# Optimization experiments

Hardware: AMD Instinct MI355X
Metric: run time of the kernel (lower is better)

The kernel has to match this reference:

```python
import jax, jax.numpy as jnp
import numpy as np

MASK_THRESHOLD = 0.01
HOTSPOT_PERCENTILE = 90.0
ALPHA = 0.5
EPS = 1e-08


def setup_inputs() -> dict:
    key = jax.random.key(0)
    k1, k2 = jax.random.split(key)
    shape = (8, 1, 128, 128, 128)  # [B, 1, D, H, W]
    pred = jax.random.uniform(k1, shape, dtype=jnp.float32)
    target = jax.random.uniform(k2, shape, dtype=jnp.float32)
    return {"pred": pred, "target": target}


def _masked_quantile(v, q):
    """Quantile (linear interpolation, matching torch.quantile) over entries v > 0.
    Falls back to MASK_THRESHOLD when no valid entries exist."""
    vv = jnp.where(v > 0, v, jnp.nan)
    th = jnp.nanquantile(vv, q)  # ignores nan entries, linear interpolation
    return jnp.where(jnp.isnan(th), jnp.asarray(MASK_THRESHOLD, v.dtype), th)


def _dice_loss_single(p, t, m):
    # p, t, m: [1, D, H, W] for one batch element
    masked_target = (t * m).ravel()
    masked_pred = (p * m).ravel()
    q = HOTSPOT_PERCENTILE / 100.0
    target_threshold = _masked_quantile(masked_target, q)
    pred_threshold = _masked_quantile(masked_pred, q)
    target_hot = (masked_target > target_threshold).astype(p.dtype)
    pred_hot = (masked_pred > pred_threshold).astype(p.dtype)
    intersection = jnp.sum(pred_hot * target_hot)
    union = jnp.sum(pred_hot) + jnp.sum(target_hot) + EPS
    return 1.0 - 2.0 * intersection / union


def reference(pred, target):
    mask = (target > MASK_THRESHOLD).astype(pred.dtype)  # [B,1,D,H,W]
    squared_error = (pred - target) ** 2 * mask
    num_valid = jnp.sum(mask, axis=(1, 2, 3, 4)) + EPS  # [B]
    mse_loss = jnp.sum(squared_error, axis=(1, 2, 3, 4)) / num_valid  # [B]
    dice_loss = jax.vmap(_dice_loss_single)(pred, target, mask)  # [B]
    combined = ALPHA * mse_loss + (1.0 - ALPHA) * dice_loss
    return jnp.mean(combined)  # reduction='mean'
```

## Files before the change

### kernel.cpp

```cpp
#include <hip/hip_runtime.h>

#define NBINS 2048
#define BPB   64
#define TPB   256
#define NB    8
#define LCAP  512
#define PCAP  8192
#define SCAP  4096

static __device__ __forceinline__ unsigned bucketOf(float v) {
    unsigned b = (unsigned)(v * (float)NBINS);
    return b > (NBINS - 1) ? (NBINS - 1) : b;
}

static __device__ __forceinline__ void gload4(float4& d, const float4* a) {
    asm volatile("global_load_dwordx4 %0, %1, off" : "=v"(d) : "v"(a));
}
#define WAIT_VMCNT(N)                                              \
    do {                                                           \
        asm volatile("s_waitcnt vmcnt(" #N ")" ::: "memory");      \
        __builtin_amdgcn_sched_barrier(0);                         \
    } while (0)

#define ISSUE(SET, c)                                              \
    do {                                                           \
        const float4* tb_ = t4 + i0 + (c) * 4 * S;                 \
        const float4* pb_ = p4 + i0 + (c) * 4 * S;                 \
        gload4(t##SET##0, tb_);         gload4(t##SET##1, tb_ + S);      \
        gload4(t##SET##2, tb_ + 2 * S); gload4(t##SET##3, tb_ + 3 * S);  \
        gload4(p##SET##0, pb_);         gload4(p##SET##1, pb_ + S);      \
        gload4(p##SET##2, pb_ + 2 * S); gload4(p##SET##3, pb_ + 3 * S);  \
    } while (0)

__global__ __launch_bounds__(TPB) void k_pass1(const float* __restrict__ pred,
                                               const float* __restrict__ targ,
                                               int nvec,
                                               unsigned short* __restrict__ hist16,
                                               double* __restrict__ sse,
                                               unsigned* __restrict__ nvalid)
{
    __shared__ unsigned h[2 * NBINS];
    for (int k = threadIdx.x; k < 2 * NBINS; k += TPB) h[k] = 0u;
    __syncthreads();

    const int b = blockIdx.y;
    const float4* __restrict__ p4 = (const float4*)pred + (size_t)b * nvec;
    const float4* __restrict__ t4 = (const float4*)targ + (size_t)b * nvec;

    float    lsse = 0.f;
    unsigned lnv = 0, lnp = 0;
    const int S  = BPB * TPB;
    const int i0 = blockIdx.x * TPB + threadIdx.x;

#define PEL1(tq, pq)                                             \
    {                                                            \
        float tv[4] = {tq.x, tq.y, tq.z, tq.w};                  \
        float pv[4] = {pq.x, pq.y, pq.z, pq.w};                  \
        _Pragma("unroll")                                        \
        for (int j = 0; j < 4; ++j) {                            \
            float tt = tv[j], pp = pv[j];                        \
            if (tt > 0.01f) {                                    \
                float d = pp - tt;                               \
                lsse += d * d; lnv++;                            \
                atomicAdd(&h[bucketOf(tt)], 1u);                 \
                if (pp > 0.f) {                                  \
                    lnp++;                                       \
                    atomicAdd(&h[NBINS + bucketOf(pp)], 1u);     \
                }                                                \
            }                                                    \
        }                                                        \
    }
#define PROC1(SET)                                               \
    {                                                            \
        PEL1(t##SET##0, p##SET##0); PEL1(t##SET##1, p##SET##1);  \
        PEL1(t##SET##2, p##SET##2); PEL1(t##SET##3, p##SET##3);  \
    }

    float4 tA0, tA1, tA2, tA3, pA0, pA1, pA2, pA3;
    float4 tB0, tB1, tB2, tB3, pB0, pB1, pB2, pB3;

    ISSUE(A, 0);
    ISSUE(B, 1); WAIT_VMCNT(8); PROC1(A);
    ISSUE(A, 2); WAIT_VMCNT(8); PROC1(B);
    ISSUE(B, 3); WAIT_VMCNT(8); PROC1(A);
    ISSUE(A, 4); WAIT_VMCNT(8); PROC1(B);
    ISSUE(B, 5); WAIT_VMCNT(8); PROC1(A);
    ISSUE(A, 6); WAIT_VMCNT(8); PROC1(B);
    ISSUE(B, 7); WAIT_VMCNT(8); PROC1(A);
    WAIT_VMCNT(0); PROC1(B);
#undef PROC1
#undef PEL1
    __syncthreads();

    unsigned short* gh = hist16 + ((size_t)b * BPB + blockIdx.x) * (2 * NBINS);
    ushort4* gh4 = (ushort4*)gh;
    for (int k = threadIdx.x; k < (2 * NBINS) / 4; k += TPB) {
        ushort4 v;
        v.x = (unsigned short)h[4 * k + 0];
        v.y = (unsigned short)h[4 * k + 1];
        v.z = (unsigned short)h[4 * k + 2];
        v.w = (unsigned short)h[4 * k + 3];
        gh4[k] = v;
    }

    for (int off = 32; off; off >>= 1) {
        lsse += __shfl_down(lsse, off);
        lnv  += __shfl_down(lnv, off);
        lnp  += __shfl_down(lnp, off);
    }
    if ((threadIdx.x & 63) == 0) {
        atomicAdd(&sse[b], (double)lsse);
        atomicAdd(&nvalid[2 * b + 0], lnv);
        atomicAdd(&nvalid[2 * b + 1], lnp);
    }
}

__global__ __launch_bounds__(256) void k_scan(const unsigned short* __restrict__ hist16,
                                              const unsigned* __restrict__ nvalid,
                                              unsigned* __restrict__ binfo)
{
    const int bt = blockIdx.x;
    const int b = bt >> 1, t = bt & 1;
    const unsigned nv = nvalid[bt];
    unsigned* bi = binfo + bt * 8;

    __shared__ unsigned partial[256];
    __shared__ unsigned sk, sr2;

    if (threadIdx.x == 0) {
        bi[5] = nv;
        if (nv == 0) {
            bi[0] = 0xFFFFFFFFu; bi[1] = 0xFFFFFFFFu;
            bi[2] = 0; bi[3] = 0; bi[4] = __float_as_uint(0.0f);
        } else {
            double pos  = 0.9 * (double)(nv - 1);
            unsigned k  = (unsigned)pos;
            double frac = pos - (double)k;
            bi[3] = k;
            bi[4] = __float_as_uint((float)frac);
            sk = k;
            sr2 = (k + 2 <= nv) ? (k + 2) : (k + 1);
        }
    }
    __syncthreads();
    if (nv == 0) return;

    const unsigned r1 = sk + 1, r2 = sr2;

    const int lo = threadIdx.x * (NBINS / 256);
    unsigned local[NBINS / 256];
#pragma unroll
    for (int j = 0; j < NBINS / 256; ++j) local[j] = 0;
    for (int rep = 0; rep < BPB; ++rep) {
        const ushort4* h4 = (const ushort4*)(hist16 +
            ((size_t)b * BPB + rep) * (2 * NBINS) + (size_t)t * NBINS + lo);
        ushort4 a = h4[0], c = h4[1];
        local[0] += a.x; local[1] += a.y; local[2] += a.z; local[3] += a.w;
        local[4] += c.x; local[5] += c.y; local[6] += c.z; local[7] += c.w;
    }
    unsigned ls = 0;
#pragma unroll
    for (int j = 0; j < NBINS / 256; ++j) ls += local[j];

    partial[threadIdx.x] = ls;
    __syncthreads();
    for (int off = 1; off < 256; off <<= 1) {
        unsigned v = (threadIdx.x >= (unsigned)off) ? partial[threadIdx.x - off] : 0u;
        __syncthreads();
        partial[threadIdx.x] += v;
        __syncthreads();
    }
    unsigned run = partial[threadIdx.x] - ls;

#pragma unroll
    for (int j = 0; j < NBINS / 256; ++j) {
        unsigned c = local[j];
        if (c) {
            if (run < r1 && run + c >= r1) { bi[0] = lo + j; bi[2] = run; }
            if (run < r2 && run + c >= r2) { bi[1] = lo + j; }
        }
        run += c;
    }
}

__global__ __launch_bounds__(TPB) void k_pass2(const float* __restrict__ pred,
                                               const float* __restrict__ targ,
                                               int nvec,
                                               const unsigned* __restrict__ binfo,
                                               unsigned* __restrict__ npairs,
                                               unsigned* __restrict__ naa,
                                               float2* __restrict__ pairs)
{
    __shared__ float2   sbuf[LCAP];
    __shared__ unsigned scnt, sbase;
    if (threadIdx.x == 0) scnt = 0;
    __syncthreads();

    const int b = blockIdx.y;
    const unsigned lo_t = binfo[(2 * b + 0) * 8 + 0], hi_t = binfo[(2 * b + 0) * 8 + 1];
    const unsigned lo_p = binfo[(2 * b + 1) * 8 + 0], hi_p = binfo[(2 * b + 1) * 8 + 1];

    const float4* __restrict__ p4 = (const float4*)pred + (size_t)b * nvec;
    const float4* __restrict__ t4 = (const float4*)targ + (size_t)b * nvec;

    unsigned laa = 0;
    const int S  = BPB * TPB;
    const int i0 = blockIdx.x * TPB + threadIdx.x;

#define PEL2(tq, pq)                                                      \
    {                                                                     \
        float tv[4] = {tq.x, tq.y, tq.z, tq.w};                           \
        float pv[4] = {pq.x, pq.y, pq.z, pq.w};                           \
        _Pragma("unroll")                                                 \
        for (int j = 0; j < 4; ++j) {                                     \
            float tt = tv[j], pp = pv[j];                                 \
            if (tt > 0.01f) {                                             \
                unsigned at = bucketOf(tt);                               \
                bool t_in = (at >= lo_t) && (at <= hi_t);                 \
                bool t_ab = (at > hi_t);                                  \
                bool ppos = (pp > 0.f);                                   \
                unsigned ap = bucketOf(pp);                               \
                bool p_in = ppos && (ap >= lo_p) && (ap <= hi_p);         \
                bool p_ab = ppos && (ap > hi_p);                          \
                if (t_ab && p_ab) laa++;                                  \
                if (t_in || p_in) {                                       \
                    unsigned idx = atomicAdd(&scnt, 1u);                  \
                    if (idx < LCAP) sbuf[idx] = make_float2(tt, pp);      \
                }                                                         \
            }                                                             \
        }                                                                 \
    }
#define PROC2(SET)                                               \
    {                                                            \
        PEL2(t##SET##0, p##SET##0); PEL2(t##SET##1, p##SET##1);  \
        PEL2(t##SET##2, p##SET##2); PEL2(t##SET##3, p##SET##3);  \
    }

    float4 tA0, tA1, tA2, tA3, pA0, pA1, pA2, pA3;
    float4 tB0, tB1, tB2, tB3, pB0, pB1, pB2, pB3;

    ISSUE(A, 0);
    ISSUE(B, 1); WAIT_VMCNT(8); PROC2(A);
    ISSUE(A, 2); WAIT_VMCNT(8); PROC2(B);
    ISSUE(B, 3); WAIT_VMCNT(8); PROC2(A);
    ISSUE(A, 4); WAIT_VMCNT(8); PROC2(B);
    ISSUE(B, 5); WAIT_VMCNT(8); PROC2(A);
    ISSUE(A, 6); WAIT_VMCNT(8); PROC2(B);
    ISSUE(B, 7); WAIT_VMCNT(8); PROC2(A);
    WAIT_VMCNT(0); PROC2(B);
#undef PROC2
#undef PEL2
    __syncthreads();
    if (threadIdx.x == 0) {
        unsigned n = scnt < LCAP ? scnt : LCAP;
        sbase = atomicAdd(&npairs[b], n);
        scnt = n;
    }
    __syncthreads();
    for (unsigned k = threadIdx.x; k < scnt; k += TPB) {
        unsigned idx = sbase + k;
        if (idx < PCAP) pairs[(size_t)b * PCAP + idx] = sbuf[k];
    }
    for (int off = 32; off; off >>= 1) laa += __shfl_down(laa, off);
    if ((threadIdx.x & 63) == 0 && laa) atomicAdd(&naa[b], laa);
}

__global__ __launch_bounds__(1024) void k_sortsel(const unsigned* __restrict__ binfo,
                                                  const unsigned* __restrict__ npairs,
                                                  const float2* __restrict__ pairs,
                                                  float* __restrict__ thr,
                                                  unsigned* __restrict__ hotc)
{
    __shared__ float s[SCAP];
    __shared__ unsigned scnt, sle;
    __shared__ float sth;

    const int bt = blockIdx.x;
    const int b = bt >> 1, t = bt & 1;
    const unsigned* bi = binfo + bt * 8;
    const unsigned nv = bi[5];
    if (nv == 0) {
        if (threadIdx.x == 0) { thr[bt] = 0.01f; hotc[bt] = 0; }
        return;
    }
    const unsigned lo = bi[0], hi = bi[1];
    if (threadIdx.x == 0) { scnt = 0; sle = 0; }
    __syncthreads();

    unsigned np = npairs[b]; if (np > PCAP) np = PCAP;
    for (unsigned i = threadIdx.x; i < np; i += 1024) {
        float2 pr = pairs[(size_t)b * PCAP + i];
        float v = t ? pr.y : pr.x;
        if (v > 0.f) {
            unsigned a = bucketOf(v);
            if (a >= lo && a <= hi) {
                unsigned idx = atomicAdd(&scnt, 1u);
                if (idx < SCAP) s[idx] = v;
            }
        }
    }
    __syncthreads();
    unsigned n = scnt < SCAP ? scnt : SCAP;
    unsigned sn = 1; while (sn < n) sn <<= 1;
    if (sn < 2) sn = 2;
    for (unsigned i = n + threadIdx.x; i < sn; i += 1024) s[i] = 3.402823466e+38f;
    __syncthreads();

    for (unsigned ksz = 2; ksz <= sn; ksz <<= 1) {
        for (unsigned j = ksz >> 1; j; j >>= 1) {
            for (unsigned i = threadIdx.x; i < sn; i += 1024) {
                unsigned ixj = i ^ j;
                if (ixj > i) {
                    float a = s[i], c = s[ixj];
                    bool up = ((i & ksz) == 0);
                    if ((a > c) == up) { s[i] = c; s[ixj] = a; }
                }
            }
            __syncthreads();
        }
    }

    if (threadIdx.x == 0) {
        unsigned k = bi[3], cb = bi[2];
        float frac = __uint_as_float(bi[4]);
        long idx = (long)k - (long)cb;
        if (idx < 0) idx = 0;
        if (idx >= (long)n) idx = (long)n - 1;
        float v0 = s[idx];
        float v1 = (idx + 1 < (long)n) ? s[idx + 1] : v0;
        sth = v0 + frac * (v1 - v0);
        thr[bt] = sth;
    }
    __syncthreads();
    float th = sth;
    unsigned cle = 0;
    for (unsigned i = threadIdx.x; i < n; i += 1024) if (s[i] <= th) cle++;
    for (int off = 32; off; off >>= 1) cle += __shfl_down(cle, off);
    if ((threadIdx.x & 63) == 0 && cle) atomicAdd(&sle, cle);
    __syncthreads();
    if (threadIdx.x == 0) {
        unsigned gle = bi[2] + sle;
        hotc[bt] = nv - gle;
    }
}

__global__ __launch_bounds__(256) void k_final(const double* __restrict__ sse,
                                               const unsigned* __restrict__ nvalid,
                                               const unsigned* __restrict__ naa,
                                               const unsigned* __restrict__ npairs,
                                               const float2* __restrict__ pairs,
                                               const float* __restrict__ thr,
                                               const unsigned* __restrict__ hotc,
                                               float* __restrict__ out)
{
    __shared__ unsigned sI;
    __shared__ double acc;
    if (threadIdx.x == 0) acc = 0.0;
    for (int b = 0; b < NB; ++b) {
        if (threadIdx.x == 0) sI = 0;
        __syncthreads();
        float th_t = thr[2 * b + 0], th_p = thr[2 * b + 1];
        unsigned np = npairs[b]; if (np > PCAP) np = PCAP;
        unsigned c = 0;
        for (unsigned i = threadIdx.x; i < np; i += 256) {
            float2 pr = pairs[(size_t)b * PCAP + i];
            if (pr.x > th_t && pr.y > th_p) c++;
        }
        for (int off = 32; off; off >>= 1) c += __shfl_down(c, off);
        if ((threadIdx.x & 63) == 0 && c) atomicAdd(&sI, c);
        __syncthreads();
        if (threadIdx.x == 0) {
            double nv  = (double)nvalid[2 * b + 0];
            double mse = sse[b] / (nv + 1e-8);
            double T = (double)hotc[2 * b + 0];
            double P = (double)hotc[2 * b + 1];
            double I = (double)(naa[b] + sI);
            double dice = 1.0 - 2.0 * I / (P + T + 1e-8);
            acc += 0.5 * mse + 0.5 * dice;
        }
        __syncthreads();
    }
    if (threadIdx.x == 0) out[0] = (float)(acc / (double)NB);
}

extern "C" void kernel_launch(void* const* d_in, const int* in_sizes, int n_in,
                              void* d_out, int out_size, void* d_ws, size_t ws_size,
                              hipStream_t stream) {
    const float* pred = (const float*)d_in[0];
    const float* targ = (const float*)d_in[1];
    float* out = (float*)d_out;

    const int total = in_sizes[0];
    const int N     = total / NB;
    const int nvec  = N / 4;

    char* ws = (char*)d_ws;
    unsigned short* hist16 = (unsigned short*)(ws + 0);
    double*   sse    = (double*)  (ws + 4194304);
    unsigned* nvalid = (unsigned*)(ws + 4194368);
    unsigned* naa    = (unsigned*)(ws + 4194432);
    unsigned* npairs = (unsigned*)(ws + 4194496);
    unsigned* binfo  = (unsigned*)(ws + 4194560);
    float*    thr    = (float*)   (ws + 4195072);
    unsigned* hotc   = (unsigned*)(ws + 4195136);
    float2*   pairs  = (float2*)  (ws + 4195200);
    (void)ws_size; (void)n_in; (void)out_size;

    hipMemsetAsync(ws + 4194304, 0, 256, stream);

    dim3 gs(BPB, NB);
    k_pass1  <<<gs, TPB, 0, stream>>>(pred, targ, nvec, hist16, sse, nvalid);
    k_scan   <<<2 * NB, 256, 0, stream>>>(hist16, nvalid, binfo);
    k_pass2  <<<gs, TPB, 0, stream>>>(pred, targ, nvec, binfo, npairs, naa, pairs);
    k_sortsel<<<2 * NB, 1024, 0, stream>>>(binfo, npairs, pairs, thr, hotc);
    k_final  <<<1, 256, 0, stream>>>(sse, nvalid, naa, npairs, pairs, thr, hotc, out);
}
```

Baseline: 180.6 us.

## Speculate quantile window to fuse histogram and compaction into one pass

Replaces the histogram pass plus the compaction pass with a single pass. That pass counts elements below, inside and above a fixed value window around the expected 90th percentile and compacts the in-window pairs. A check kernel confirms that the quantile rank falls inside the window. Otherwise the original histogram, scan and compaction path runs as a fallback, so correctness holds for any input. This removes one full read of both input volumes in the common case, at the cost of extra small kernel launches, a guessed window, and a larger pair buffer.

```diff
diff --git a/kernel.cpp b/kernel.cpp
--- a/kernel.cpp
+++ b/kernel.cpp
@@ -4,9 +4,15 @@
 #define BPB   64
 #define TPB   256
 #define NB    8
-#define LCAP  512
-#define PCAP  8192
-#define SCAP  4096
+
+#define WLO 0.89453125f
+#define WHI 0.90673828125f
+
+#define PCAP  57344
+#define LCAP  1536
+#define FB_PCAP 8192
+#define FB_LCAP 512
+#define CCAP  512
 
 static __device__ __forceinline__ unsigned bucketOf(float v) {
     unsigned b = (unsigned)(v * (float)NBINS);
@@ -22,25 +28,39 @@
         __builtin_amdgcn_sched_barrier(0);                         \
     } while (0)
 
-#define ISSUE(SET, c)                                              \
-    do {                                                           \
-        const float4* tb_ = t4 + i0 + (c) * 4 * S;                 \
-        const float4* pb_ = p4 + i0 + (c) * 4 * S;                 \
+#define ISSUE(SET, c)                                                    \
+    do {                                                                 \
+        const float4* tb_ = t4 + i0 + (c) * 4 * S;                       \
+        const float4* pb_ = p4 + i0 + (c) * 4 * S;                       \
         gload4(t##SET##0, tb_);         gload4(t##SET##1, tb_ + S);      \
         gload4(t##SET##2, tb_ + 2 * S); gload4(t##SET##3, tb_ + 3 * S);  \
         gload4(p##SET##0, pb_);         gload4(p##SET##1, pb_ + S);      \
         gload4(p##SET##2, pb_ + 2 * S); gload4(p##SET##3, pb_ + 3 * S);  \
     } while (0)
 
-__global__ __launch_bounds__(TPB) void k_pass1(const float* __restrict__ pred,
-                                               const float* __restrict__ targ,
-                                               int nvec,
-                                               unsigned short* __restrict__ hist16,
-                                               double* __restrict__ sse,
-                                               unsigned* __restrict__ nvalid)
-{
-    __shared__ unsigned h[2 * NBINS];
-    for (int k = threadIdx.x; k < 2 * NBINS; k += TPB) h[k] = 0u;
+#define PIPELINE8(PROC)                      \
+    ISSUE(A, 0);                             \
+    ISSUE(B, 1); WAIT_VMCNT(8); PROC(A);     \
+    ISSUE(A, 2); WAIT_VMCNT(8); PROC(B);     \
+    ISSUE(B, 3); WAIT_VMCNT(8); PROC(A);     \
+    ISSUE(A, 4); WAIT_VMCNT(8); PROC(B);     \
+    ISSUE(B, 5); WAIT_VMCNT(8); PROC(A);     \
+    ISSUE(A, 6); WAIT_VMCNT(8); PROC(B);     \
+    ISSUE(B, 7); WAIT_VMCNT(8); PROC(A);     \
+    WAIT_VMCNT(0); PROC(B);
+
+
+__global__ __launch_bounds__(TPB) void k_main(const float* __restrict__ pred,
+                                              const float* __restrict__ targ,
+                                              int nvec,
+                                              double* __restrict__ sse,
+                                              unsigned* __restrict__ cnt,
+                                              unsigned* __restrict__ oflow,
+                                              float2* __restrict__ pairs)
+{
+    __shared__ float2   sbuf[LCAP];
+    __shared__ unsigned scnt, sbase;
+    if (threadIdx.x == 0) scnt = 0;
     __syncthreads();
 
     const int b = blockIdx.y;
@@ -48,11 +68,139 @@
     const float4* __restrict__ t4 = (const float4*)targ + (size_t)b * nvec;
 
     float    lsse = 0.f;
-    unsigned lnv = 0, lnp = 0;
+    unsigned lnvt = 0, lnvp = 0, linwt = 0, linwp = 0, labvt = 0, labvp = 0, lnaa = 0;
     const int S  = BPB * TPB;
     const int i0 = blockIdx.x * TPB + threadIdx.x;
 
-#define PEL1(tq, pq)                                             \
+#define PELM(tq, pq)                                                         \
+    {                                                                        \
+        float tv[4] = {tq.x, tq.y, tq.z, tq.w};                              \
+        float pv[4] = {pq.x, pq.y, pq.z, pq.w};                              \
+        _Pragma("unroll")                                                    \
+        for (int j = 0; j < 4; ++j) {                                        \
+            float tt = tv[j], pp = pv[j];                                    \
+            if (tt > 0.01f) {                                                \
+                float d = pp - tt;                                           \
+                lsse += d * d; lnvt++;                                       \
+                bool pz = (pp > 0.f); if (pz) lnvp++;                        \
+                bool tin = (tt >= WLO) && (tt < WHI);                        \
+                bool pin = pz && (pp >= WLO) && (pp < WHI);                  \
+                bool tab = (tt >= WHI);                                      \
+                bool pab = (pp >= WHI);                                      \
+                if (tin) linwt++;                                            \
+                if (pin) linwp++;                                            \
+                if (tab) labvt++;                                            \
+                if (pab) labvp++;                                            \
+                if (tab && pab) lnaa++;                                      \
+                if (tin || pin) {                                            \
+                    unsigned idx = atomicAdd(&scnt, 1u);                     \
+                    if (idx < LCAP) sbuf[idx] = make_float2(tt, pp);         \
+                }                                                            \
+            }                                                                \
+        }                                                                    \
+    }
+#define PROCM(SET)                                               \
+    {                                                            \
+        PELM(t##SET##0, p##SET##0); PELM(t##SET##1, p##SET##1);  \
+        PELM(t##SET##2, p##SET##2); PELM(t##SET##3, p##SET##3);  \
+    }
+
+    float4 tA0, tA1, tA2, tA3, pA0, pA1, pA2, pA3;
+    float4 tB0, tB1, tB2, tB3, pB0, pB1, pB2, pB3;
+    PIPELINE8(PROCM)
+#undef PROCM
+#undef PELM
+    __syncthreads();
+
+    if (threadIdx.x == 0) {
+        unsigned n = scnt;
+        if (n > LCAP) { atomicOr(oflow, 1u); n = LCAP; }
+        sbase = atomicAdd(&cnt[b * 8 + 7], n);
+        scnt = n;
+    }
+    __syncthreads();
+    for (unsigned k = threadIdx.x; k < scnt; k += TPB) {
+        unsigned idx = sbase + k;
+        if (idx < PCAP) pairs[(size_t)b * PCAP + idx] = sbuf[k];
+    }
+
+    for (int off = 32; off; off >>= 1) {
+        lsse  += __shfl_down(lsse, off);
+        lnvt  += __shfl_down(lnvt, off);
+        lnvp  += __shfl_down(lnvp, off);
+        linwt += __shfl_down(linwt, off);
+        linwp += __shfl_down(linwp, off);
+        labvt += __shfl_down(labvt, off);
+        labvp += __shfl_down(labvp, off);
+        lnaa  += __shfl_down(lnaa, off);
+    }
+    if ((threadIdx.x & 63) == 0) {
+        atomicAdd(&sse[b], (double)lsse);
+        atomicAdd(&cnt[b * 8 + 0], lnvt);
+        atomicAdd(&cnt[b * 8 + 1], lnvp);
+        atomicAdd(&cnt[b * 8 + 2], linwt);
+        atomicAdd(&cnt[b * 8 + 3], linwp);
+        atomicAdd(&cnt[b * 8 + 4], labvt);
+        atomicAdd(&cnt[b * 8 + 5], labvp);
+        atomicAdd(&cnt[b * 8 + 6], lnaa);
+    }
+}
+
+__global__ __launch_bounds__(64) void k_check(const unsigned* __restrict__ cnt,
+                                              const unsigned* __restrict__ oflow,
+                                              unsigned* __restrict__ sinfo)
+{
+    __shared__ unsigned okarr[16];
+    const int bt = threadIdx.x;
+    if (bt < 16) {
+        const int b = bt >> 1, t = bt & 1;
+        unsigned nv  = cnt[b * 8 + t];
+        unsigned inW = cnt[b * 8 + 2 + t];
+        unsigned abv = cnt[b * 8 + 4 + t];
+        unsigned below = nv - inW - abv;
+        unsigned ok = 0, k = 0; float frac = 0.f;
+        if (nv > 0 && inW > 0) {
+            double pos = 0.9 * (double)(nv - 1);
+            k = (unsigned)pos;
+            frac = (float)(pos - (double)k);
+            if (k >= below && (k + 1) <= below + inW - 1) ok = 1;
+        }
+        if (cnt[b * 8 + 7] > PCAP) ok = 0;
+        if (*oflow) ok = 0;
+        unsigned* si = sinfo + 8 + bt * 8;
+        si[0] = k;
+        si[1] = __float_as_uint(frac);
+        si[2] = below;
+        si[3] = nv;
+        si[4] = abv;
+        okarr[bt] = ok;
+    }
+    __syncthreads();
+    if (threadIdx.x == 0) {
+        unsigned ok = 1;
+        for (int i = 0; i < 16; ++i) ok &= okarr[i];
+        sinfo[0] = ok;
+    }
+}
+
+__global__ __launch_bounds__(TPB) void k_hist_fb(const float* __restrict__ pred,
+                                                 const float* __restrict__ targ,
+                                                 int nvec,
+                                                 const unsigned* __restrict__ sinfo,
+                                                 unsigned short* __restrict__ hist16)
+{
+    if (sinfo[0]) return;
+    __shared__ unsigned h[2 * NBINS];
+    for (int k = threadIdx.x; k < 2 * NBINS; k += TPB) h[k] = 0u;
+    __syncthreads();
+
+    const int b = blockIdx.y;
+    const float4* __restrict__ p4 = (const float4*)pred + (size_t)b * nvec;
+    const float4* __restrict__ t4 = (const float4*)targ + (size_t)b * nvec;
+    const int S  = BPB * TPB;
+    const int i0 = blockIdx.x * TPB + threadIdx.x;
+
+#define PELH(tq, pq)                                             \
     {                                                            \
         float tv[4] = {tq.x, tq.y, tq.z, tq.w};                  \
         float pv[4] = {pq.x, pq.y, pq.z, pq.w};                  \
@@ -60,36 +208,22 @@
         for (int j = 0; j < 4; ++j) {                            \
             float tt = tv[j], pp = pv[j];                        \
             if (tt > 0.01f) {                                    \
-                float d = pp - tt;                               \
-                lsse += d * d; lnv++;                            \
                 atomicAdd(&h[bucketOf(tt)], 1u);                 \
-                if (pp > 0.f) {                                  \
-                    lnp++;                                       \
+                if (pp > 0.f)                                    \
                     atomicAdd(&h[NBINS + bucketOf(pp)], 1u);     \
-                }                                                \
             }                                                    \
         }                                                        \
     }
-#define PROC1(SET)                                               \
+#define PROCH(SET)                                               \
     {                                                            \
-        PEL1(t##SET##0, p##SET##0); PEL1(t##SET##1, p##SET##1);  \
-        PEL1(t##SET##2, p##SET##2); PEL1(t##SET##3, p##SET##3);  \
-    }
-
+        PELH(t##SET##0, p##SET##0); PELH(t##SET##1, p##SET##1);  \
+        PELH(t##SET##2, p##SET##2); PELH(t##SET##3, p##SET##3);  \
+    }
     float4 tA0, tA1, tA2, tA3, pA0, pA1, pA2, pA3;
     float4 tB0, tB1, tB2, tB3, pB0, pB1, pB2, pB3;
-
-    ISSUE(A, 0);
-    ISSUE(B, 1); WAIT_VMCNT(8); PROC1(A);
-    ISSUE(A, 2); WAIT_VMCNT(8); PROC1(B);
-    ISSUE(B, 3); WAIT_VMCNT(8); PROC1(A);
-    ISSUE(A, 4); WAIT_VMCNT(8); PROC1(B);
-    ISSUE(B, 5); WAIT_VMCNT(8); PROC1(A);
-    ISSUE(A, 6); WAIT_VMCNT(8); PROC1(B);
-    ISSUE(B, 7); WAIT_VMCNT(8); PROC1(A);
-    WAIT_VMCNT(0); PROC1(B);
-#undef PROC1
-#undef PEL1
+    PIPELINE8(PROCH)
+#undef PROCH
+#undef PELH
     __syncthreads();
 
     unsigned short* gh = hist16 + ((size_t)b * BPB + blockIdx.x) * (2 * NBINS);
@@ -102,26 +236,17 @@
         v.w = (unsigned short)h[4 * k + 3];
         gh4[k] = v;
     }
-
-    for (int off = 32; off; off >>= 1) {
-        lsse += __shfl_down(lsse, off);
-        lnv  += __shfl_down(lnv, off);
-        lnp  += __shfl_down(lnp, off);
-    }
-    if ((threadIdx.x & 63) == 0) {
-        atomicAdd(&sse[b], (double)lsse);
-        atomicAdd(&nvalid[2 * b + 0], lnv);
-        atomicAdd(&nvalid[2 * b + 1], lnp);
-    }
-}
-
-__global__ __launch_bounds__(256) void k_scan(const unsigned short* __restrict__ hist16,
-                                              const unsigned* __restrict__ nvalid,
-                                              unsigned* __restrict__ binfo)
-{
+}
+
+__global__ __launch_bounds__(256) void k_scan_fb(const unsigned short* __restrict__ hist16,
+                                                 const unsigned* __restrict__ cnt,
+                                                 const unsigned* __restrict__ sinfo,
+                                                 unsigned* __restrict__ binfo)
+{
+    if (sinfo[0]) return;
     const int bt = blockIdx.x;
     const int b = bt >> 1, t = bt & 1;
-    const unsigned nv = nvalid[bt];
+    const unsigned nv = cnt[b * 8 + t];
     unsigned* bi = binfo + bt * 8;
 
     __shared__ unsigned partial[256];
@@ -135,9 +260,8 @@
         } else {
             double pos  = 0.9 * (double)(nv - 1);
             unsigned k  = (unsigned)pos;
-            double frac = pos - (double)k;
             bi[3] = k;
-            bi[4] = __float_as_uint((float)frac);
+            bi[4] = __float_as_uint((float)(pos - (double)k));
             sk = k;
             sr2 = (k + 2 <= nv) ? (k + 2) : (k + 1);
         }
@@ -146,7 +270,6 @@
     if (nv == 0) return;
 
     const unsigned r1 = sk + 1, r2 = sr2;
-
     const int lo = threadIdx.x * (NBINS / 256);
     unsigned local[NBINS / 256];
 #pragma unroll
@@ -161,7 +284,6 @@
     unsigned ls = 0;
 #pragma unroll
     for (int j = 0; j < NBINS / 256; ++j) ls += local[j];
-
     partial[threadIdx.x] = ls;
     __syncthreads();
     for (int off = 1; off < 256; off <<= 1) {
@@ -171,7 +293,6 @@
         __syncthreads();
     }
     unsigned run = partial[threadIdx.x] - ls;
-
 #pragma unroll
     for (int j = 0; j < NBINS / 256; ++j) {
         unsigned c = local[j];
@@ -183,15 +304,17 @@
     }
 }
 
-__global__ __launch_bounds__(TPB) void k_pass2(const float* __restrict__ pred,
-                                               const float* __restrict__ targ,
-                                               int nvec,
-                                               const unsigned* __restrict__ binfo,
-                                               unsigned* __restrict__ npairs,
-                                               unsigned* __restrict__ naa,
-                                               float2* __restrict__ pairs)
-{
-    __shared__ float2   sbuf[LCAP];
+__global__ __launch_bounds__(TPB) void k_compact_fb(const float* __restrict__ pred,
+                                                    const float* __restrict__ targ,
+                                                    int nvec,
+                                                    const unsigned* __restrict__ sinfo,
+                                                    const unsigned* __restrict__ binfo,
+                                                    unsigned* __restrict__ fb_npairs,
+                                                    unsigned* __restrict__ fb_naa,
+                                                    float2* __restrict__ fb_pairs)
+{
+    if (sinfo[0]) return;
+    __shared__ float2   sbuf[FB_LCAP];
     __shared__ unsigned scnt, sbase;
     if (threadIdx.x == 0) scnt = 0;
     __syncthreads();
@@ -202,12 +325,11 @@
 
     const float4* __restrict__ p4 = (const float4*)pred + (size_t)b * nvec;
     const float4* __restrict__ t4 = (const float4*)targ + (size_t)b * nvec;
-
     unsigned laa = 0;
     const int S  = BPB * TPB;
     const int i0 = blockIdx.x * TPB + threadIdx.x;
 
-#define PEL2(tq, pq)                                                      \
+#define PELC(tq, pq)                                                      \
     {                                                                     \
         float tv[4] = {tq.x, tq.y, tq.z, tq.w};                           \
         float pv[4] = {pq.x, pq.y, pq.z, pq.w};                           \
@@ -225,162 +347,228 @@
                 if (t_ab && p_ab) laa++;                                  \
                 if (t_in || p_in) {                                       \
                     unsigned idx = atomicAdd(&scnt, 1u);                  \
-                    if (idx < LCAP) sbuf[idx] = make_float2(tt, pp);      \
+                    if (idx < FB_LCAP) sbuf[idx] = make_float2(tt, pp);   \
                 }                                                         \
             }                                                             \
         }                                                                 \
     }
-#define PROC2(SET)                                               \
+#define PROCC(SET)                                               \
     {                                                            \
-        PEL2(t##SET##0, p##SET##0); PEL2(t##SET##1, p##SET##1);  \
-        PEL2(t##SET##2, p##SET##2); PEL2(t##SET##3, p##SET##3);  \
-    }
-
+        PELC(t##SET##0, p##SET##0); PELC(t##SET##1, p##SET##1);  \
+        PELC(t##SET##2, p##SET##2); PELC(t##SET##3, p##SET##3);  \
+    }
     float4 tA0, tA1, tA2, tA3, pA0, pA1, pA2, pA3;
     float4 tB0, tB1, tB2, tB3, pB0, pB1, pB2, pB3;
-
-    ISSUE(A, 0);
-    ISSUE(B, 1); WAIT_VMCNT(8); PROC2(A);
-    ISSUE(A, 2); WAIT_VMCNT(8); PROC2(B);
-    ISSUE(B, 3); WAIT_VMCNT(8); PROC2(A);
-    ISSUE(A, 4); WAIT_VMCNT(8); PROC2(B);
-    ISSUE(B, 5); WAIT_VMCNT(8); PROC2(A);
-    ISSUE(A, 6); WAIT_VMCNT(8); PROC2(B);
-    ISSUE(B, 7); WAIT_VMCNT(8); PROC2(A);
-    WAIT_VMCNT(0); PROC2(B);
-#undef PROC2
-#undef PEL2
+    PIPELINE8(PROCC)
+#undef PROCC
+#undef PELC
     __syncthreads();
     if (threadIdx.x == 0) {
-        unsigned n = scnt < LCAP ? scnt : LCAP;
-        sbase = atomicAdd(&npairs[b], n);
+        unsigned n = scnt < FB_LCAP ? scnt : FB_LCAP;
+        sbase = atomicAdd(&fb_npairs[b], n);
         scnt = n;
     }
     __syncthreads();
     for (unsigned k = threadIdx.x; k < scnt; k += TPB) {
         unsigned idx = sbase + k;
-        if (idx < PCAP) pairs[(size_t)b * PCAP + idx] = sbuf[k];
+        if (idx < FB_PCAP) fb_pairs[(size_t)b * FB_PCAP + idx] = sbuf[k];
     }
     for (int off = 32; off; off >>= 1) laa += __shfl_down(laa, off);
-    if ((threadIdx.x & 63) == 0 && laa) atomicAdd(&naa[b], laa);
-}
-
-__global__ __launch_bounds__(1024) void k_sortsel(const unsigned* __restrict__ binfo,
-                                                  const unsigned* __restrict__ npairs,
-                                                  const float2* __restrict__ pairs,
-                                                  float* __restrict__ thr,
-                                                  unsigned* __restrict__ hotc)
-{
-    __shared__ float s[SCAP];
-    __shared__ unsigned scnt, sle;
-    __shared__ float sth;
+    if ((threadIdx.x & 63) == 0 && laa) atomicAdd(&fb_naa[b], laa);
+}
+
+__global__ __launch_bounds__(1024) void k_select(const unsigned* __restrict__ sinfo,
+                                                 const unsigned* __restrict__ cnt,
+                                                 const float2* __restrict__ pairs,
+                                                 const unsigned* __restrict__ binfo,
+                                                 const unsigned* __restrict__ fb_npairs,
+                                                 const float2* __restrict__ fb_pairs,
+                                                 float* __restrict__ thr,
+                                                 unsigned* __restrict__ hotc)
+{
+    __shared__ unsigned hc[2048];
+    __shared__ unsigned partial[1024];
+    __shared__ float    sv[CCAP];
+    __shared__ unsigned sb_lo, sb_hi, scc, scle;
+    __shared__ float    sth;
 
     const int bt = blockIdx.x;
     const int b = bt >> 1, t = bt & 1;
-    const unsigned* bi = binfo + bt * 8;
-    const unsigned nv = bi[5];
-    if (nv == 0) {
-        if (threadIdx.x == 0) { thr[bt] = 0.01f; hotc[bt] = 0; }
-        return;
-    }
-    const unsigned lo = bi[0], hi = bi[1];
-    if (threadIdx.x == 0) { scnt = 0; sle = 0; }
-    __syncthreads();
-
-    unsigned np = npairs[b]; if (np > PCAP) np = PCAP;
+    const unsigned ok = sinfo[0];
+
+    unsigned k, below, nv;
+    float frac, rlo, rhi;
+    unsigned blo_bk = 0, bhi_bk = 0;
+    const float2* src;
+    unsigned np;
+
+    if (ok) {
+        const unsigned* si = sinfo + 8 + bt * 8;
+        k = si[0]; frac = __uint_as_float(si[1]); below = si[2]; nv = si[3];
+        rlo = WLO; rhi = WHI;
+        src = pairs + (size_t)b * PCAP;
+        np = cnt[b * 8 + 7]; if (np > PCAP) np = PCAP;
+    } else {
+        const unsigned* bi = binfo + bt * 8;
+        nv = bi[5];
+        if (nv == 0) {
+            if (threadIdx.x == 0) { thr[bt] = 0.01f; hotc[bt] = 0; }
+            return;
+        }
+        blo_bk = bi[0]; bhi_bk = bi[1]; below = bi[2]; k = bi[3];
+        frac = __uint_as_float(bi[4]);
+        rlo = (float)blo_bk * (1.0f / NBINS);
+        rhi = (float)(bhi_bk + 1) * (1.0f / NBINS);
+        src = fb_pairs + (size_t)b * FB_PCAP;
+        np = fb_npairs[b]; if (np > FB_PCAP) np = FB_PCAP;
+    }
+    const float scale = 2048.0f / (rhi - rlo);
+
+#define MEMB(v) (ok ? ((v) >= WLO && (v) < WHI)                                   \
+                    : ((v) > 0.f && bucketOf(v) >= blo_bk && bucketOf(v) <= bhi_bk))
+
+    for (int i = threadIdx.x; i < 2048; i += 1024) hc[i] = 0u;
+    if (threadIdx.x == 0) { sb_lo = 0xFFFFFFFFu; sb_hi = 0xFFFFFFFFu; scc = 0; scle = 0; }
+    __syncthreads();
+
     for (unsigned i = threadIdx.x; i < np; i += 1024) {
-        float2 pr = pairs[(size_t)b * PCAP + i];
+        float2 pr = src[i];
         float v = t ? pr.y : pr.x;
-        if (v > 0.f) {
-            unsigned a = bucketOf(v);
-            if (a >= lo && a <= hi) {
-                unsigned idx = atomicAdd(&scnt, 1u);
-                if (idx < SCAP) s[idx] = v;
+        if (MEMB(v)) {
+            int bin = (int)((v - rlo) * scale);
+            bin = bin < 0 ? 0 : (bin > 2047 ? 2047 : bin);
+            atomicAdd(&hc[bin], 1u);
+        }
+    }
+    __syncthreads();
+
+    unsigned h0 = hc[2 * threadIdx.x], h1 = hc[2 * threadIdx.x + 1];
+    unsigned ssum = h0 + h1;
+    partial[threadIdx.x] = ssum;
+    __syncthreads();
+    for (int off = 1; off < 1024; off <<= 1) {
+        unsigned v = (threadIdx.x >= (unsigned)off) ? partial[threadIdx.x - off] : 0u;
+        __syncthreads();
+        partial[threadIdx.x] += v;
+        __syncthreads();
+    }
+    unsigned excl = partial[threadIdx.x] - ssum;
+    hc[2 * threadIdx.x]     = excl + h0;
+    hc[2 * threadIdx.x + 1] = excl + ssum;
+    __syncthreads();
+
+    const unsigned r  = k - below;
+    const unsigned r1 = r + 1, r2 = r + 2;
+    for (int j = 2 * threadIdx.x; j <= 2 * threadIdx.x + 1; ++j) {
+        unsigned c = hc[j];
+        unsigned prev = (j == 0) ? 0u : hc[j - 1];
+        if (c >= r1 && prev < r1) atomicMin(&sb_lo, (unsigned)j);
+        if (c >= r2 && prev < r2) atomicMin(&sb_hi, (unsigned)j);
+    }
+    __syncthreads();
+    unsigned b_lo = sb_lo, b_hi = sb_hi;
+    if (b_hi == 0xFFFFFFFFu) b_hi = 2047;
+    if (b_lo == 0xFFFFFFFFu) b_lo = 2047;
+    unsigned cumlo = (b_lo > 0) ? hc[b_lo - 1] : 0u;
+
+    for (unsigned i = threadIdx.x; i < np; i += 1024) {
+        float2 pr = src[i];
+        float v = t ? pr.y : pr.x;
+        if (MEMB(v)) {
+            int bin = (int)((v - rlo) * scale);
+            bin = bin < 0 ? 0 : (bin > 2047 ? 2047 : bin);
+            if ((unsigned)bin >= b_lo && (unsigned)bin <= b_hi) {
+                unsigned idx = atomicAdd(&scc, 1u);
+                if (idx < CCAP) sv[idx] = v;
             }
         }
     }
     __syncthreads();
-    unsigned n = scnt < SCAP ? scnt : SCAP;
-    unsigned sn = 1; while (sn < n) sn <<= 1;
-    if (sn < 2) sn = 2;
-    for (unsigned i = n + threadIdx.x; i < sn; i += 1024) s[i] = 3.402823466e+38f;
-    __syncthreads();
-
-    for (unsigned ksz = 2; ksz <= sn; ksz <<= 1) {
-        for (unsigned j = ksz >> 1; j; j >>= 1) {
-            for (unsigned i = threadIdx.x; i < sn; i += 1024) {
-                unsigned ixj = i ^ j;
-                if (ixj > i) {
-                    float a = s[i], c = s[ixj];
-                    bool up = ((i & ksz) == 0);
-                    if ((a > c) == up) { s[i] = c; s[ixj] = a; }
-                }
-            }
-            __syncthreads();
+    unsigned n_cmp = scc < CCAP ? scc : CCAP;
+
+    for (unsigned ph = 0; ph < n_cmp; ++ph) {
+        unsigned idx = 2 * threadIdx.x + (ph & 1);
+        if (idx + 1 < n_cmp) {
+            float a = sv[idx], c = sv[idx + 1];
+            if (a > c) { sv[idx] = c; sv[idx + 1] = a; }
         }
+        __syncthreads();
     }
 
     if (threadIdx.x == 0) {
-        unsigned k = bi[3], cb = bi[2];
-        float frac = __uint_as_float(bi[4]);
-        long idx = (long)k - (long)cb;
-        if (idx < 0) idx = 0;
-        if (idx >= (long)n) idx = (long)n - 1;
-        float v0 = s[idx];
-        float v1 = (idx + 1 < (long)n) ? s[idx + 1] : v0;
+        long rl = (long)r - (long)cumlo;
+        if (rl < 0) rl = 0;
+        if (rl >= (long)n_cmp) rl = (long)n_cmp - 1;
+        float v0 = sv[rl];
+        float v1 = (rl + 1 < (long)n_cmp) ? sv[rl + 1] : v0;
         sth = v0 + frac * (v1 - v0);
         thr[bt] = sth;
     }
     __syncthreads();
     float th = sth;
+
     unsigned cle = 0;
-    for (unsigned i = threadIdx.x; i < n; i += 1024) if (s[i] <= th) cle++;
+    for (unsigned i = threadIdx.x; i < np; i += 1024) {
+        float2 pr = src[i];
+        float v = t ? pr.y : pr.x;
+        if (MEMB(v) && v <= th) cle++;
+    }
     for (int off = 32; off; off >>= 1) cle += __shfl_down(cle, off);
-    if ((threadIdx.x & 63) == 0 && cle) atomicAdd(&sle, cle);
+    if ((threadIdx.x & 63) == 0 && cle) atomicAdd(&scle, cle);
+    __syncthreads();
+    if (threadIdx.x == 0) hotc[bt] = nv - below - scle;
+#undef MEMB
+}
+
+__global__ __launch_bounds__(256) void k_resolve(const unsigned* __restrict__ sinfo,
+                                                 const double* __restrict__ sse,
+                                                 const unsigned* __restrict__ cnt,
+                                                 const float2* __restrict__ pairs,
+                                                 const unsigned* __restrict__ fb_npairs,
+                                                 const unsigned* __restrict__ fb_naa,
+                                                 const float2* __restrict__ fb_pairs,
+                                                 const float* __restrict__ thr,
+                                                 const unsigned* __restrict__ hotc,
+                                                 double* __restrict__ loss_part)
+{
+    __shared__ unsigned sI;
+    if (threadIdx.x == 0) sI = 0;
+    __syncthreads();
+    const int b = blockIdx.x;
+    const unsigned ok = sinfo[0];
+    const float2* src = ok ? (pairs + (size_t)b * PCAP) : (fb_pairs + (size_t)b * FB_PCAP);
+    unsigned np  = ok ? cnt[b * 8 + 7] : fb_npairs[b];
+    unsigned cap = ok ? PCAP : FB_PCAP;
+    if (np > cap) np = cap;
+    unsigned naa = ok ? cnt[b * 8 + 6] : fb_naa[b];
+
+    float th_t = thr[2 * b + 0], th_p = thr[2 * b + 1];
+    unsigned c = 0;
+    for (unsigned i = threadIdx.x; i < np; i += 256) {
+        float2 pr = src[i];
+        if (pr.x > th_t && pr.y > th_p) c++;
+    }
+    for (int off = 32; off; off >>= 1) c += __shfl_down(c, off);
+    if ((threadIdx.x & 63) == 0 && c) atomicAdd(&sI, c);
     __syncthreads();
     if (threadIdx.x == 0) {
-        unsigned gle = bi[2] + sle;
-        hotc[bt] = nv - gle;
-    }
-}
-
-__global__ __launch_bounds__(256) void k_final(const double* __restrict__ sse,
-                                               const unsigned* __restrict__ nvalid,
-                                               const unsigned* __restrict__ naa,
-                                               const unsigned* __restrict__ npairs,
-                                               const float2* __restrict__ pairs,
-                                               const float* __restrict__ thr,
-                                               const unsigned* __restrict__ hotc,
-                                               float* __restrict__ out)
-{
-    __shared__ unsigned sI;
-    __shared__ double acc;
-    if (threadIdx.x == 0) acc = 0.0;
-    for (int b = 0; b < NB; ++b) {
-        if (threadIdx.x == 0) sI = 0;
-        __syncthreads();
-        float th_t = thr[2 * b + 0], th_p = thr[2 * b + 1];
-        unsigned np = npairs[b]; if (np > PCAP) np = PCAP;
-        unsigned c = 0;
-        for (unsigned i = threadIdx.x; i < np; i += 256) {
-            float2 pr = pairs[(size_t)b * PCAP + i];
-            if (pr.x > th_t && pr.y > th_p) c++;
-        }
-        for (int off = 32; off; off >>= 1) c += __shfl_down(c, off);
-        if ((threadIdx.x & 63) == 0 && c) atomicAdd(&sI, c);
-        __syncthreads();
-        if (threadIdx.x == 0) {
-            double nv  = (double)nvalid[2 * b + 0];
-            double mse = sse[b] / (nv + 1e-8);
-            double T = (double)hotc[2 * b + 0];
-            double P = (double)hotc[2 * b + 1];
-            double I = (double)(naa[b] + sI);
-            double dice = 1.0 - 2.0 * I / (P + T + 1e-8);
-            acc += 0.5 * mse + 0.5 * dice;
-        }
-        __syncthreads();
-    }
-    if (threadIdx.x == 0) out[0] = (float)(acc / (double)NB);
+        double nv  = (double)cnt[b * 8 + 0];
+        double mse = sse[b] / (nv + 1e-8);
+        double T = (double)hotc[2 * b + 0];
+        double P = (double)hotc[2 * b + 1];
+        double I = (double)(naa + sI);
+        double dice = 1.0 - 2.0 * I / (P + T + 1e-8);
+        loss_part[b] = 0.5 * mse + 0.5 * dice;
+    }
+}
+
+__global__ void k_final(const double* __restrict__ loss_part, float* __restrict__ out)
+{
+    if (threadIdx.x == 0 && blockIdx.x == 0) {
+        double acc = 0.0;
+        for (int b = 0; b < NB; ++b) acc += loss_part[b];
+        out[0] = (float)(acc / (double)NB);
+    }
 }
 
 extern "C" void kernel_launch(void* const* d_in, const int* in_sizes, int n_in,
@@ -395,23 +583,30 @@
     const int nvec  = N / 4;
 
     char* ws = (char*)d_ws;
+    float2*         pairs  = (float2*)(ws + 0);
     unsigned short* hist16 = (unsigned short*)(ws + 0);
-    double*   sse    = (double*)  (ws + 4194304);
-    unsigned* nvalid = (unsigned*)(ws + 4194368);
-    unsigned* naa    = (unsigned*)(ws + 4194432);
-    unsigned* npairs = (unsigned*)(ws + 4194496);
-    unsigned* binfo  = (unsigned*)(ws + 4194560);
-    float*    thr    = (float*)   (ws + 4195072);
-    unsigned* hotc   = (unsigned*)(ws + 4195136);
-    float2*   pairs  = (float2*)  (ws + 4195200);
+    double*   sse       = (double*)  (ws + 4194304);
+    unsigned* cnt       = (unsigned*)(ws + 4194368);
+    unsigned* oflow     = (unsigned*)(ws + 4194624);
+    unsigned* fb_naa    = (unsigned*)(ws + 4194688);
+    unsigned* fb_npairs = (unsigned*)(ws + 4194752);
+    double*   loss_part = (double*)  (ws + 4194816);
+    unsigned* sinfo     = (unsigned*)(ws + 4194880);
+    unsigned* binfo     = (unsigned*)(ws + 4195904);
+    float*    thr       = (float*)   (ws + 4196416);
+    unsigned* hotc      = (unsigned*)(ws + 4196480);
+    float2*   fb_pairs  = (float2*)  (ws + 4196544);
     (void)ws_size; (void)n_in; (void)out_size;
 
-    hipMemsetAsync(ws + 4194304, 0, 256, stream);
+    hipMemsetAsync(ws + 4194304, 0, 512, stream);
 
     dim3 gs(BPB, NB);
-    k_pass1  <<<gs, TPB, 0, stream>>>(pred, targ, nvec, hist16, sse, nvalid);
-    k_scan   <<<2 * NB, 256, 0, stream>>>(hist16, nvalid, binfo);
-    k_pass2  <<<gs, TPB, 0, stream>>>(pred, targ, nvec, binfo, npairs, naa, pairs);
-    k_sortsel<<<2 * NB, 1024, 0, stream>>>(binfo, npairs, pairs, thr, hotc);
-    k_final  <<<1, 256, 0, stream>>>(sse, nvalid, naa, npairs, pairs, thr, hotc, out);
-}
+    k_main      <<<gs, TPB, 0, stream>>>(pred, targ, nvec, sse, cnt, oflow, pairs);
+    k_check     <<<1, 64, 0, stream>>>(cnt, oflow, sinfo);
+    k_hist_fb   <<<gs, TPB, 0, stream>>>(pred, targ, nvec, sinfo, hist16);
+    k_scan_fb   <<<2 * NB, 256, 0, stream>>>(hist16, cnt, sinfo, binfo);
+    k_compact_fb<<<gs, TPB, 0, stream>>>(pred, targ, nvec, sinfo, binfo, fb_npairs, fb_naa, fb_pairs);
+    k_select    <<<2 * NB, 1024, 0, stream>>>(sinfo, cnt, pairs, binfo, fb_npairs, fb_pairs, thr, hotc);
+    k_resolve   <<<NB, 256, 0, stream>>>(sinfo, sse, cnt, pairs, fb_npairs, fb_naa, fb_pairs, thr, hotc, loss_part);
+    k_final     <<<1, 64, 0, stream>>>(loss_part, out);
+}
```

New measurement: 233.9 us. +29.5%, slower.
